# Optimization experiments

Hardware: AMD Instinct MI355X
Metric: run time of the kernel (lower is better)

## Reference

```python
import jax, jax.numpy as jnp
import numpy as np

NEG = -9.0e9  # the -9000000000.0 sentinel used by the torch code


def _masked_bidir_scores(first, second, fmask, smask):
    """Vectorized form of the BxB python double loop in score_grounding.
    first: (B,N,D), second: (B,L,D), fmask: (B,N), smask: (B,L).
    Returns sent_scores (B,B) and mention_scores (B,N,L) (= diagonal att)."""
    mask = fmask[:, None, :, None] * smask[None, :, None, :]          # (B,B,N,L)
    avg = jnp.where(mask != 0, mask, NEG)
    am_first = jax.nn.softmax(avg, axis=2)                            # softmax over N (dim=0 per pair)
    am_second = jax.nn.softmax(avg, axis=3)                           # softmax over L (dim=1 per pair)
    dot = jnp.einsum('ind,jld->ijnl', first, second)                  # (B,B,N,L)
    attm = dot * mask
    att = jnp.where(attm * mask != 0, attm, NEG)
    aw_first = jax.nn.softmax(att, axis=3) * mask                     # softmax(att, dim=-1)*mask
    aw_second = jnp.transpose(
        jax.nn.softmax(jnp.swapaxes(att, 2, 3), axis=3) * jnp.swapaxes(mask, 2, 3), (0, 1, 3, 2)
    )                                                                 # softmax(att.T,-1)*mask.T, transposed back
    sent = (jnp.sum(aw_first * att * am_first, axis=(2, 3))
            + jnp.sum(aw_second * att * am_second, axis=(2, 3)))      # (B,B)
    B = first.shape[0]
    mention = att[jnp.arange(B), jnp.arange(B)]                       # diagonal pairs (B,N,L)
    return sent, mention


def _pairwise_mlp(first, second, W1, b1, W2, b2, W3, b3):
    # SimplePairWiseClassifier: MLP over cat(first, second, first*second); dropout=0 (eval-deterministic)
    x = jnp.concatenate([first, second, first * second], axis=-1)     # (..., 3D)
    h = jax.nn.relu(x @ W1 + b1)
    h = jax.nn.relu(h @ W2 + b2)
    return (h @ W3 + b3)[..., 0]


def setup_inputs() -> dict:
    key = jax.random.key(0)
    ks = jax.random.split(key, 12)
    B, Nt, Ns, L, D, H = 32, 64, 48, 36, 1024, 1024

    def mask(k, n):
        m = (jax.random.uniform(k, (B, n)) < 0.85).astype(jnp.float32)
        return m.at[:, :2].set(1.0)  # guarantee no all-zero rows

    return {
        'text_embeddings': jax.random.normal(ks[0], (B, Nt, D), jnp.float32),
        'span_embeddings': jax.random.normal(ks[1], (B, Ns, D), jnp.float32),
        'image_embeddings': jax.random.normal(ks[2], (B, L, D), jnp.float32),
        'text_mask': mask(ks[3], Nt),
        'span_mask': mask(ks[4], Ns),
        'image_mask': mask(ks[5], L),
        'W1': jax.random.normal(ks[6], (3 * D, H), jnp.float32) * 0.02,
        'b1': jnp.zeros((H,), jnp.float32),
        'W2': jax.random.normal(ks[7], (H, H), jnp.float32) * 0.02,
        'b2': jnp.zeros((H,), jnp.float32),
        'W3': jax.random.normal(ks[8], (H, 1), jnp.float32) * 0.02,
        'b3': jnp.zeros((1,), jnp.float32),
    }


def reference(text_embeddings, span_embeddings, image_embeddings,
              text_mask, span_mask, image_mask, W1, b1, W2, b2, W3, b3):
    B, Ns, D = span_embeddings.shape
    # calculate_loss
    S, _ = _masked_bidir_scores(text_embeddings, image_embeddings, text_mask, image_mask)
    # span_emb.view(B, N, -1, D).mean(dim=2) is identity for (B,Ns,D)
    _, grounding_scores = _masked_bidir_scores(span_embeddings, image_embeddings, span_mask, image_mask)
    # score_text over all span pairs (itertools.combinations order == triu_indices k=1)
    fi, si = np.triu_indices(Ns, k=1)
    text_scores = _pairwise_mlp(span_embeddings[:, fi], span_embeddings[:, si],
                                W1, b1, W2, b2, W3, b3)               # (B, Ns*(Ns-1)/2)
    # contrastive retrieval loss over the BxB sentence-image score matrix
    loss = -(jnp.trace(jax.nn.log_softmax(S, axis=1))
             + jnp.trace(jax.nn.log_softmax(S.T, axis=1))) / B
    return loss, grounding_scores, text_scores
```

## Files before the change

kernel.cpp:

```cpp
#include <hip/hip_runtime.h>
#include <math.h>
#include <stdint.h>

#define B_    32
#define NT    64
#define NS    48
#define LI    36
#define D_    1024
#define H_    1024
#define NPAIR 1128
#define ROWS  (B_*NPAIR)
#define NEGV  -9.0e9f

typedef _Float16 half8 __attribute__((ext_vector_type(8)));
typedef float floatx4 __attribute__((ext_vector_type(4)));
typedef __attribute__((address_space(3))) uint32_t lds_u32;
typedef __attribute__((address_space(1))) const uint32_t glb_u32;

template<int EPI>
__global__ __launch_bounds__(256) void mfma_gemm(
    const _Float16* __restrict__ A, const _Float16* __restrict__ Bt,
    float* __restrict__ Cf, float* __restrict__ scores,
    const float* __restrict__ bias, const float* __restrict__ W3,
    int N, int K, int rowStart) {
  __shared__ __align__(16) _Float16 sA[128 * 32];
  __shared__ __align__(16) _Float16 sB[128 * 32];
  __shared__ float sRed[128][2];
  const int tid = threadIdx.x;
  const int lane = tid & 63;
  const int wave = tid >> 6;
  const int wr = wave >> 1, wc = wave & 1;
  const int l15 = lane & 15, l16 = lane >> 4;
  const int rowBase = blockIdx.y * 128, colBase = blockIdx.x * 128;

  const int stRow = tid >> 2;
  const int stCol = (tid & 3) << 3;
  const _Float16* gA = A + (size_t)(rowBase + stRow) * K + stCol;
  const _Float16* gB = Bt + (size_t)(colBase + stRow) * K + stCol;
  _Float16* lA = sA + tid * 8;
  _Float16* lB = sB + tid * 8;

  floatx4 acc[4][4] = {};
  for (int k0 = 0; k0 < K; k0 += 32) {
    __builtin_amdgcn_global_load_lds((glb_u32*)(gA + k0),           (lds_u32*)lA,             16, 0, 0);
    __builtin_amdgcn_global_load_lds((glb_u32*)(gA + 64 * K + k0),  (lds_u32*)(lA + 64 * 32), 16, 0, 0);
    __builtin_amdgcn_global_load_lds((glb_u32*)(gB + k0),           (lds_u32*)lB,             16, 0, 0);
    __builtin_amdgcn_global_load_lds((glb_u32*)(gB + 64 * K + k0),  (lds_u32*)(lB + 64 * 32), 16, 0, 0);
    __syncthreads();
    half8 aF[4], bF[4];
#pragma unroll
    for (int i = 0; i < 4; ++i)
      aF[i] = *(const half8*)&sA[(wr * 64 + i * 16 + l15) * 32 + l16 * 8];
#pragma unroll
    for (int j = 0; j < 4; ++j)
      bF[j] = *(const half8*)&sB[(wc * 64 + j * 16 + l15) * 32 + l16 * 8];
#pragma unroll
    for (int i = 0; i < 4; ++i)
#pragma unroll
      for (int j = 0; j < 4; ++j)
        acc[i][j] = __builtin_amdgcn_mfma_f32_16x16x32_f16(aF[i], bF[j], acc[i][j], 0, 0, 0);
    __syncthreads();
  }

  if (EPI == 0) {
#pragma unroll
    for (int i = 0; i < 4; ++i)
#pragma unroll
      for (int q = 0; q < 4; ++q) {
        int r = rowBase + wr * 64 + i * 16 + l16 * 4 + q;
#pragma unroll
        for (int j = 0; j < 4; ++j) {
          int c = colBase + wc * 64 + j * 16 + l15;
          Cf[(size_t)r * N + c] = acc[i][j][q];
        }
      }
  } else {
    float bv[4], wv[4];
#pragma unroll
    for (int j = 0; j < 4; ++j) {
      int c = colBase + wc * 64 + j * 16 + l15;
      bv[j] = bias[c];
      wv[j] = W3[c];
    }
#pragma unroll
    for (int i = 0; i < 4; ++i)
#pragma unroll
      for (int q = 0; q < 4; ++q) {
        float s = 0.f;
#pragma unroll
        for (int j = 0; j < 4; ++j) s += fmaxf(acc[i][j][q] + bv[j], 0.f) * wv[j];
        s += __shfl_xor(s, 1); s += __shfl_xor(s, 2);
        s += __shfl_xor(s, 4); s += __shfl_xor(s, 8);
        if (l15 == 0) sRed[wr * 64 + i * 16 + l16 * 4 + q][wc] = s;
      }
    __syncthreads();
    if (tid < 128)
      atomicAdd(&scores[rowStart + rowBase + tid], sRed[tid][0] + sRed[tid][1]);
  }
}

__global__ __launch_bounds__(256) void gemm1_fused(
    const _Float16* __restrict__ spanH, const _Float16* __restrict__ W1cT,
    const float* __restrict__ AB1, const float* __restrict__ b1,
    _Float16* __restrict__ h1out,
    const int* __restrict__ idxF, const int* __restrict__ idxS) {
  __shared__ __align__(16) _Float16 sA[128 * 32];
  __shared__ __align__(16) _Float16 sB[128 * 32];
  __shared__ int sIF[128], sIS[128];
  const int tid = threadIdx.x;
  const int lane = tid & 63;
  const int wave = tid >> 6;
  const int wr = wave >> 1, wc = wave & 1;
  const int l15 = lane & 15, l16 = lane >> 4;
  const int rowBase = blockIdx.y * 128, colBase = blockIdx.x * 128;

  if (tid < 128) {
    int rg = rowBase + tid;
    sIF[tid] = idxF[rg];
    sIS[tid] = idxS[rg];
  }
  __syncthreads();

  const int stRow = tid >> 2;
  const int stCol = (tid & 3) << 3;
  const _Float16* gB = W1cT + (size_t)(colBase + stRow) * D_ + stCol;
  _Float16* lB = sB + tid * 8;
  const size_t pf0 = (size_t)sIF[stRow] * D_;
  const size_t ps0 = (size_t)sIS[stRow] * D_;
  const size_t pf1 = (size_t)sIF[stRow + 64] * D_;
  const size_t ps1 = (size_t)sIS[stRow + 64] * D_;

  floatx4 acc[4][4] = {};
  for (int k0 = 0; k0 < D_; k0 += 32) {
    __builtin_amdgcn_global_load_lds((glb_u32*)(gB + k0),           (lds_u32*)lB,             16, 0, 0);
    __builtin_amdgcn_global_load_lds((glb_u32*)(gB + 64 * D_ + k0), (lds_u32*)(lB + 64 * 32), 16, 0, 0);
    half8 f0 = *(const half8*)(spanH + pf0 + k0 + stCol);
    half8 s0 = *(const half8*)(spanH + ps0 + k0 + stCol);
    half8 f1 = *(const half8*)(spanH + pf1 + k0 + stCol);
    half8 s1 = *(const half8*)(spanH + ps1 + k0 + stCol);
    *(half8*)(sA + stRow * 32 + stCol) = f0 * s0;
    *(half8*)(sA + (stRow + 64) * 32 + stCol) = f1 * s1;
    __syncthreads();
    half8 aF[4], bF[4];
#pragma unroll
    for (int i = 0; i < 4; ++i)
      aF[i] = *(const half8*)&sA[(wr * 64 + i * 16 + l15) * 32 + l16 * 8];
#pragma unroll
    for (int j = 0; j < 4; ++j)
      bF[j] = *(const half8*)&sB[(wc * 64 + j * 16 + l15) * 32 + l16 * 8];
#pragma unroll
    for (int i = 0; i < 4; ++i)
#pragma unroll
      for (int j = 0; j < 4; ++j)
        acc[i][j] = __builtin_amdgcn_mfma_f32_16x16x32_f16(aF[i], bF[j], acc[i][j], 0, 0, 0);
    __syncthreads();
  }

  int cols[4]; float bv[4];
#pragma unroll
  for (int j = 0; j < 4; ++j) {
    cols[j] = colBase + wc * 64 + j * 16 + l15;
    bv[j] = b1[cols[j]];
  }
#pragma unroll
  for (int i = 0; i < 4; ++i)
#pragma unroll
    for (int q = 0; q < 4; ++q) {
      int rL = wr * 64 + i * 16 + l16 * 4 + q;
      int rG = rowBase + rL;
      const float* ap = AB1 + (size_t)sIF[rL] * 2048;
      const float* bp = AB1 + (size_t)sIS[rL] * 2048 + 1024;
#pragma unroll
      for (int j = 0; j < 4; ++j) {
        int c = cols[j];
        float v = acc[i][j][q] + ap[c] + bp[c] + bv[j];
        h1out[(size_t)rG * 1024 + c] = (_Float16)fmaxf(v, 0.f);
      }
    }
}

__global__ __launch_bounds__(256) void cvt_f16(
    const float* __restrict__ in, _Float16* __restrict__ out, long long n8) {
  long long i = (long long)blockIdx.x * 256 + threadIdx.x;
  if (i >= n8) return;
  const float4* p = (const float4*)in + i * 2;
  float4 a = p[0], b = p[1];
  half8 h;
  h[0] = (_Float16)a.x; h[1] = (_Float16)a.y; h[2] = (_Float16)a.z; h[3] = (_Float16)a.w;
  h[4] = (_Float16)b.x; h[5] = (_Float16)b.y; h[6] = (_Float16)b.z; h[7] = (_Float16)b.w;
  *(half8*)(out + i * 8) = h;
}

__global__ __launch_bounds__(256) void transpose_cvt(
    const float* __restrict__ in, _Float16* __restrict__ out) {
  __shared__ float t[32][33];
  const int tx = threadIdx.x & 31, ty = threadIdx.x >> 5;
  const int k0 = blockIdx.y * 32, n0 = blockIdx.x * 32;
#pragma unroll
  for (int q = 0; q < 4; ++q)
    t[ty + q * 8][tx] = in[(size_t)(k0 + ty + q * 8) * 1024 + n0 + tx];
  __syncthreads();
#pragma unroll
  for (int q = 0; q < 4; ++q)
    out[(size_t)(n0 + ty + q * 8) * 1024 + k0 + tx] = (_Float16)t[tx][ty + q * 8];
}

__global__ __launch_bounds__(256) void idx_init(int* __restrict__ idxF, int* __restrict__ idxS) {
  int r = blockIdx.x * 256 + threadIdx.x;
  if (r >= ROWS) return;
  int bb = r / NPAIR, p = r - bb * NPAIR;
  int cum = 0, f = 0;
  while (true) { int cnt = NS - 1 - f; if (p < cum + cnt) break; cum += cnt; ++f; }
  idxF[r] = bb * NS + f;
  idxS[r] = bb * NS + f + 1 + (p - cum);
}

__global__ void init_scores(float* __restrict__ scores, const float* __restrict__ b3) {
  int idx = blockIdx.x * 256 + threadIdx.x;
  if (idx < ROWS) scores[idx] = b3[0];
}

__global__ __launch_bounds__(256) void extract_grounding(
    const float* __restrict__ dotSI, const float* __restrict__ smask,
    const float* __restrict__ imask, float* __restrict__ outg) {
  int idx = blockIdx.x * 256 + threadIdx.x;
  if (idx >= B_ * NS * LI) return;
  int b = idx / (NS * LI);
  int rem = idx - b * (NS * LI);
  int n = rem / LI, l = rem - n * LI;
  float v = dotSI[(size_t)(b * NS + n) * (B_ * LI) + b * LI + l];
  outg[idx] = (smask[b * NS + n] * imask[b * LI + l] != 0.f) ? v : NEGV;
}

__global__ __launch_bounds__(64) void sent_kernel(
    const float* __restrict__ dotTI, const float* __restrict__ tmask,
    const float* __restrict__ imask, float* __restrict__ S) {
  const int i = blockIdx.y, j = blockIdx.x, t = threadIdx.x;
  __shared__ float red1[64], red2[64];
  const int stride = B_ * LI;
  float e1 = 0.f;
  {
    float tm = tmask[i * NT + t];
    if (tm != 0.f) {
      const float* row = dotTI + (size_t)(i * NT + t) * stride + j * LI;
      float m = -INFINITY;
      for (int l = 0; l < LI; ++l) if (imask[j * LI + l] != 0.f) m = fmaxf(m, row[l]);
      float z = 0.f, w = 0.f;
      for (int l = 0; l < LI; ++l) if (imask[j * LI + l] != 0.f) {
        float d = row[l], p = expf(d - m);
        z += p; w += p * d;
      }
      e1 = w / z;
    }
  }
  red1[t] = e1;
  float e2 = 0.f;
  if (t < LI) {
    float im = imask[j * LI + t];
    if (im != 0.f) {
      const float* col = dotTI + (size_t)(i * NT) * stride + j * LI + t;
      float m = -INFINITY;
      for (int n = 0; n < NT; ++n) if (tmask[i * NT + n] != 0.f) m = fmaxf(m, col[(size_t)n * stride]);
      float z = 0.f, w = 0.f;
      for (int n = 0; n < NT; ++n) if (tmask[i * NT + n] != 0.f) {
        float d = col[(size_t)n * stride], p = expf(d - m);
        z += p; w += p * d;
      }
      e2 = w / z;
    }
  }
  red2[t] = e2;
  __syncthreads();
  if (t == 0) {
    float s1 = 0.f, s2 = 0.f, cn = 0.f, cl = 0.f;
    for (int n = 0; n < NT; ++n) { s1 += red1[n]; cn += tmask[i * NT + n]; }
    for (int l = 0; l < LI; ++l) { s2 += red2[l]; cl += imask[j * LI + l]; }
    S[i * B_ + j] = s1 / cn + s2 / cl;
  }
}

__global__ __launch_bounds__(64) void loss_kernel(
    const float* __restrict__ S, float* __restrict__ out) {
  __shared__ float sS[B_][B_ + 1];
  __shared__ float acc[B_];
  const int t = threadIdx.x;
  for (int e = t; e < B_ * B_; e += 64) sS[e / B_][e % B_] = S[e];
  __syncthreads();
  if (t < B_) {
    float m = -INFINITY;
    for (int j = 0; j < B_; ++j) m = fmaxf(m, sS[t][j]);
    float z = 0.f;
    for (int j = 0; j < B_; ++j) z += expf(sS[t][j] - m);
    float lr = m + logf(z);
    float m2 = -INFINITY;
    for (int i = 0; i < B_; ++i) m2 = fmaxf(m2, sS[i][t]);
    float z2 = 0.f;
    for (int i = 0; i < B_; ++i) z2 += expf(sS[i][t] - m2);
    float lc = m2 + logf(z2);
    acc[t] = 2.f * sS[t][t] - lr - lc;
  }
  __syncthreads();
  if (t == 0) {
    float s = 0.f;
    for (int i = 0; i < B_; ++i) s += acc[i];
    out[0] = -s / (float)B_;
  }
}

extern "C" void kernel_launch(void* const* d_in, const int* in_sizes, int n_in,
                              void* d_out, int out_size, void* d_ws, size_t ws_size,
                              hipStream_t stream) {
  const float* text  = (const float*)d_in[0];
  const float* span  = (const float*)d_in[1];
  const float* img   = (const float*)d_in[2];
  const float* tmask = (const float*)d_in[3];
  const float* smask = (const float*)d_in[4];
  const float* imask = (const float*)d_in[5];
  const float* W1    = (const float*)d_in[6];
  const float* b1    = (const float*)d_in[7];
  const float* W2    = (const float*)d_in[8];
  const float* b2    = (const float*)d_in[9];
  const float* W3    = (const float*)d_in[10];
  const float* b3    = (const float*)d_in[11];

  float* out     = (float*)d_out;
  float* outLoss = out;
  float* outG    = out + 1;
  float* outT    = out + 1 + (size_t)B_ * NS * LI;

  char* w = (char*)d_ws;
  float*    dotTI = (float*)w;            w += (size_t)(B_*NT) * (B_*LI) * 4;
  float*    dotSI = (float*)w;            w += (size_t)(B_*NS) * (B_*LI) * 4;
  float*    S     = (float*)w;            w += 1024 * 4;
  float*    AB1   = (float*)w;            w += (size_t)1536 * 2048 * 4;
  _Float16* h1    = (_Float16*)w;         w += (size_t)ROWS * 1024 * 2;
  _Float16* textH = (_Float16*)w;         w += (size_t)2048 * 1024 * 2;
  _Float16* spanH = (_Float16*)w;         w += (size_t)1536 * 1024 * 2;
  _Float16* imgH  = (_Float16*)w;         w += (size_t)1152 * 1024 * 2;
  _Float16* W1abT = (_Float16*)w;         w += (size_t)2048 * 1024 * 2;
  _Float16* W1cT  = (_Float16*)w;         w += (size_t)1024 * 1024 * 2;
  _Float16* W2T   = (_Float16*)w;         w += (size_t)1024 * 1024 * 2;
  int*      idxF  = (int*)w;              w += ROWS * 4;
  int*      idxS  = (int*)w;              w += ROWS * 4;
  (void)ws_size; (void)in_sizes; (void)n_in; (void)out_size;

  cvt_f16<<<(2048 * 128 + 255) / 256, 256, 0, stream>>>(text, textH, 2048LL * 128);
  cvt_f16<<<(1536 * 128 + 255) / 256, 256, 0, stream>>>(span, spanH, 1536LL * 128);
  cvt_f16<<<(1152 * 128 + 255) / 256, 256, 0, stream>>>(img, imgH, 1152LL * 128);
  transpose_cvt<<<dim3(32, 32), 256, 0, stream>>>(W1, W1abT);
  transpose_cvt<<<dim3(32, 32), 256, 0, stream>>>(W1 + 1024 * 1024, W1abT + 1024 * 1024);
  transpose_cvt<<<dim3(32, 32), 256, 0, stream>>>(W1 + 2048 * 1024, W1cT);
  transpose_cvt<<<dim3(32, 32), 256, 0, stream>>>(W2, W2T);
  idx_init<<<(ROWS + 255) / 256, 256, 0, stream>>>(idxF, idxS);

  mfma_gemm<0><<<dim3((B_*LI) / 128, (B_*NT) / 128), 256, 0, stream>>>(
      textH, imgH, dotTI, nullptr, nullptr, nullptr, B_ * LI, D_, 0);
  sent_kernel<<<dim3(B_, B_), 64, 0, stream>>>(dotTI, tmask, imask, S);
  loss_kernel<<<1, 64, 0, stream>>>(S, outLoss);

  mfma_gemm<0><<<dim3((B_*LI) / 128, (B_*NS) / 128), 256, 0, stream>>>(
      spanH, imgH, dotSI, nullptr, nullptr, nullptr, B_ * LI, D_, 0);
  extract_grounding<<<(B_*NS*LI + 255) / 256, 256, 0, stream>>>(dotSI, smask, imask, outG);

  mfma_gemm<0><<<dim3(2048 / 128, 1536 / 128), 256, 0, stream>>>(
      spanH, W1abT, AB1, nullptr, nullptr, nullptr, 2048, D_, 0);

  gemm1_fused<<<dim3(1024 / 128, ROWS / 128), 256, 0, stream>>>(
      spanH, W1cT, AB1, b1, h1, idxF, idxS);

  init_scores<<<(ROWS + 255) / 256, 256, 0, stream>>>(outT, b3);
  mfma_gemm<2><<<dim3(1024 / 128, ROWS / 128), 256, 0, stream>>>(
      h1, W2T, nullptr, outT, b2, W3, 1024, H_, 0);
}
```

Measured before the change: 385.9 us.

## Double K-step per barrier and remap blocks to XCD-contiguous row tiles

GEMM main loops now load a 64-wide K slab per iteration as two 32-wide halves, halving the number of barriers and load-issue rounds per tile. The two large MLP GEMMs switch to a 1D grid whose block IDs are remapped so each XCD processes a contiguous band of row tiles across all column tiles, aiming to improve L2 locality of the A operand. LDS use per block doubles, which may reduce occupancy, and a few padding blocks exit early.

```diff
diff --git a/kernel.cpp b/kernel.cpp
--- a/kernel.cpp
+++ b/kernel.cpp
@@ -11,54 +11,76 @@
 #define NPAIR 1128
 #define ROWS  (B_*NPAIR)
 #define NEGV  -9.0e9f
+#define NROWT 282
+#define CPX   36
 
 typedef _Float16 half8 __attribute__((ext_vector_type(8)));
 typedef float floatx4 __attribute__((ext_vector_type(4)));
 typedef __attribute__((address_space(3))) uint32_t lds_u32;
 typedef __attribute__((address_space(1))) const uint32_t glb_u32;
 
-template<int EPI>
+#define GLOAD16(src, dst) __builtin_amdgcn_global_load_lds((glb_u32*)(src), (lds_u32*)(dst), 16, 0, 0)
+
+template<int EPI, int REMAP>
 __global__ __launch_bounds__(256) void mfma_gemm(
     const _Float16* __restrict__ A, const _Float16* __restrict__ Bt,
     float* __restrict__ Cf, float* __restrict__ scores,
     const float* __restrict__ bias, const float* __restrict__ W3,
-    int N, int K, int rowStart) {
-  __shared__ __align__(16) _Float16 sA[128 * 32];
-  __shared__ __align__(16) _Float16 sB[128 * 32];
+    int N, int K) {
+  __shared__ __align__(16) _Float16 sA[8192];
+  __shared__ __align__(16) _Float16 sB[8192];
   __shared__ float sRed[128][2];
+  int rowT, colT;
+  if (REMAP) {
+    int bid = blockIdx.x;
+    int x = bid & 7, ord = bid >> 3;
+    rowT = x * CPX + (ord >> 3);
+    colT = ord & 7;
+    if (rowT >= NROWT) return;
+  } else {
+    rowT = blockIdx.y; colT = blockIdx.x;
+  }
+  const int rowBase = rowT * 128, colBase = colT * 128;
   const int tid = threadIdx.x;
   const int lane = tid & 63;
   const int wave = tid >> 6;
   const int wr = wave >> 1, wc = wave & 1;
   const int l15 = lane & 15, l16 = lane >> 4;
-  const int rowBase = blockIdx.y * 128, colBase = blockIdx.x * 128;
-
-  const int stRow = tid >> 2;
-  const int stCol = (tid & 3) << 3;
-  const _Float16* gA = A + (size_t)(rowBase + stRow) * K + stCol;
-  const _Float16* gB = Bt + (size_t)(colBase + stRow) * K + stCol;
+
+  const int sRow = tid >> 2;
+  const int sCol = (tid & 3) << 3;
+  const _Float16* gA = A + (size_t)(rowBase + sRow) * K + sCol;
+  const _Float16* gB = Bt + (size_t)(colBase + sRow) * K + sCol;
   _Float16* lA = sA + tid * 8;
   _Float16* lB = sB + tid * 8;
 
   floatx4 acc[4][4] = {};
-  for (int k0 = 0; k0 < K; k0 += 32) {
-    __builtin_amdgcn_global_load_lds((glb_u32*)(gA + k0),           (lds_u32*)lA,             16, 0, 0);
-    __builtin_amdgcn_global_load_lds((glb_u32*)(gA + 64 * K + k0),  (lds_u32*)(lA + 64 * 32), 16, 0, 0);
-    __builtin_amdgcn_global_load_lds((glb_u32*)(gB + k0),           (lds_u32*)lB,             16, 0, 0);
-    __builtin_amdgcn_global_load_lds((glb_u32*)(gB + 64 * K + k0),  (lds_u32*)(lB + 64 * 32), 16, 0, 0);
+  for (int k0 = 0; k0 < K; k0 += 64) {
+    GLOAD16(gA + k0,              lA);
+    GLOAD16(gA + 64 * K + k0,     lA + 2048);
+    GLOAD16(gA + k0 + 32,         lA + 4096);
+    GLOAD16(gA + 64 * K + k0 + 32,lA + 6144);
+    GLOAD16(gB + k0,              lB);
+    GLOAD16(gB + 64 * K + k0,     lB + 2048);
+    GLOAD16(gB + k0 + 32,         lB + 4096);
+    GLOAD16(gB + 64 * K + k0 + 32,lB + 6144);
     __syncthreads();
-    half8 aF[4], bF[4];
-#pragma unroll
-    for (int i = 0; i < 4; ++i)
-      aF[i] = *(const half8*)&sA[(wr * 64 + i * 16 + l15) * 32 + l16 * 8];
-#pragma unroll
-    for (int j = 0; j < 4; ++j)
-      bF[j] = *(const half8*)&sB[(wc * 64 + j * 16 + l15) * 32 + l16 * 8];
-#pragma unroll
-    for (int i = 0; i < 4; ++i)
+#pragma unroll
+    for (int h = 0; h < 2; ++h) {
+      const int hb = h * 4096;
+      half8 aF[4], bF[4];
+#pragma unroll
+      for (int i = 0; i < 4; ++i)
+        aF[i] = *(const half8*)&sA[hb + (wr * 64 + i * 16 + l15) * 32 + l16 * 8];
 #pragma unroll
       for (int j = 0; j < 4; ++j)
-        acc[i][j] = __builtin_amdgcn_mfma_f32_16x16x32_f16(aF[i], bF[j], acc[i][j], 0, 0, 0);
+        bF[j] = *(const half8*)&sB[hb + (wc * 64 + j * 16 + l15) * 32 + l16 * 8];
+#pragma unroll
+      for (int i = 0; i < 4; ++i)
+#pragma unroll
+        for (int j = 0; j < 4; ++j)
+          acc[i][j] = __builtin_amdgcn_mfma_f32_16x16x32_f16(aF[i], bF[j], acc[i][j], 0, 0, 0);
+    }
     __syncthreads();
   }
 
@@ -95,7 +117,7 @@
       }
     __syncthreads();
     if (tid < 128)
-      atomicAdd(&scores[rowStart + rowBase + tid], sRed[tid][0] + sRed[tid][1]);
+      atomicAdd(&scores[rowBase + tid], sRed[tid][0] + sRed[tid][1]);
   }
 }
 
@@ -104,15 +126,20 @@
     const float* __restrict__ AB1, const float* __restrict__ b1,
     _Float16* __restrict__ h1out,
     const int* __restrict__ idxF, const int* __restrict__ idxS) {
-  __shared__ __align__(16) _Float16 sA[128 * 32];
-  __shared__ __align__(16) _Float16 sB[128 * 32];
+  __shared__ __align__(16) _Float16 sA[8192];
+  __shared__ __align__(16) _Float16 sB[8192];
   __shared__ int sIF[128], sIS[128];
+  int bid = blockIdx.x;
+  int x = bid & 7, ord = bid >> 3;
+  int rowT = x * CPX + (ord >> 3);
+  int colT = ord & 7;
+  if (rowT >= NROWT) return;
+  const int rowBase = rowT * 128, colBase = colT * 128;
   const int tid = threadIdx.x;
   const int lane = tid & 63;
   const int wave = tid >> 6;
   const int wr = wave >> 1, wc = wave & 1;
   const int l15 = lane & 15, l16 = lane >> 4;
-  const int rowBase = blockIdx.y * 128, colBase = blockIdx.x * 128;
 
   if (tid < 128) {
     int rg = rowBase + tid;
@@ -121,38 +148,50 @@
   }
   __syncthreads();
 
-  const int stRow = tid >> 2;
-  const int stCol = (tid & 3) << 3;
-  const _Float16* gB = W1cT + (size_t)(colBase + stRow) * D_ + stCol;
+  const int sRow = tid >> 2;
+  const int sCol = (tid & 3) << 3;
+  const _Float16* gB = W1cT + (size_t)(colBase + sRow) * D_ + sCol;
   _Float16* lB = sB + tid * 8;
-  const size_t pf0 = (size_t)sIF[stRow] * D_;
-  const size_t ps0 = (size_t)sIS[stRow] * D_;
-  const size_t pf1 = (size_t)sIF[stRow + 64] * D_;
-  const size_t ps1 = (size_t)sIS[stRow + 64] * D_;
+  const _Float16* pf0 = spanH + (size_t)sIF[sRow] * D_ + sCol;
+  const _Float16* ps0 = spanH + (size_t)sIS[sRow] * D_ + sCol;
+  const _Float16* pf1 = spanH + (size_t)sIF[sRow + 64] * D_ + sCol;
+  const _Float16* ps1 = spanH + (size_t)sIS[sRow + 64] * D_ + sCol;
 
   floatx4 acc[4][4] = {};
-  for (int k0 = 0; k0 < D_; k0 += 32) {
-    __builtin_amdgcn_global_load_lds((glb_u32*)(gB + k0),           (lds_u32*)lB,             16, 0, 0);
-    __builtin_amdgcn_global_load_lds((glb_u32*)(gB + 64 * D_ + k0), (lds_u32*)(lB + 64 * 32), 16, 0, 0);
-    half8 f0 = *(const half8*)(spanH + pf0 + k0 + stCol);
-    half8 s0 = *(const half8*)(spanH + ps0 + k0 + stCol);
-    half8 f1 = *(const half8*)(spanH + pf1 + k0 + stCol);
-    half8 s1 = *(const half8*)(spanH + ps1 + k0 + stCol);
-    *(half8*)(sA + stRow * 32 + stCol) = f0 * s0;
-    *(half8*)(sA + (stRow + 64) * 32 + stCol) = f1 * s1;
+  for (int k0 = 0; k0 < D_; k0 += 64) {
+    GLOAD16(gB + k0,               lB);
+    GLOAD16(gB + 64 * D_ + k0,     lB + 2048);
+    GLOAD16(gB + k0 + 32,          lB + 4096);
+    GLOAD16(gB + 64 * D_ + k0 + 32,lB + 6144);
+    half8 f00 = *(const half8*)(pf0 + k0);
+    half8 s00 = *(const half8*)(ps0 + k0);
+    half8 f10 = *(const half8*)(pf1 + k0);
+    half8 s10 = *(const half8*)(ps1 + k0);
+    half8 f01 = *(const half8*)(pf0 + k0 + 32);
+    half8 s01 = *(const half8*)(ps0 + k0 + 32);
+    half8 f11 = *(const half8*)(pf1 + k0 + 32);
+    half8 s11 = *(const half8*)(ps1 + k0 + 32);
+    *(half8*)(sA + tid * 8)        = f00 * s00;
+    *(half8*)(sA + 2048 + tid * 8) = f10 * s10;
+    *(half8*)(sA + 4096 + tid * 8) = f01 * s01;
+    *(half8*)(sA + 6144 + tid * 8) = f11 * s11;
     __syncthreads();
-    half8 aF[4], bF[4];
-#pragma unroll
-    for (int i = 0; i < 4; ++i)
-      aF[i] = *(const half8*)&sA[(wr * 64 + i * 16 + l15) * 32 + l16 * 8];
-#pragma unroll
-    for (int j = 0; j < 4; ++j)
-      bF[j] = *(const half8*)&sB[(wc * 64 + j * 16 + l15) * 32 + l16 * 8];
-#pragma unroll
-    for (int i = 0; i < 4; ++i)
+#pragma unroll
+    for (int h = 0; h < 2; ++h) {
+      const int hb = h * 4096;
+      half8 aF[4], bF[4];
+#pragma unroll
+      for (int i = 0; i < 4; ++i)
+        aF[i] = *(const half8*)&sA[hb + (wr * 64 + i * 16 + l15) * 32 + l16 * 8];
 #pragma unroll
       for (int j = 0; j < 4; ++j)
-        acc[i][j] = __builtin_amdgcn_mfma_f32_16x16x32_f16(aF[i], bF[j], acc[i][j], 0, 0, 0);
+        bF[j] = *(const half8*)&sB[hb + (wc * 64 + j * 16 + l15) * 32 + l16 * 8];
+#pragma unroll
+      for (int i = 0; i < 4; ++i)
+#pragma unroll
+        for (int j = 0; j < 4; ++j)
+          acc[i][j] = __builtin_amdgcn_mfma_f32_16x16x32_f16(aF[i], bF[j], acc[i][j], 0, 0, 0);
+    }
     __syncthreads();
   }
 
@@ -353,22 +392,22 @@
   transpose_cvt<<<dim3(32, 32), 256, 0, stream>>>(W2, W2T);
   idx_init<<<(ROWS + 255) / 256, 256, 0, stream>>>(idxF, idxS);
 
-  mfma_gemm<0><<<dim3((B_*LI) / 128, (B_*NT) / 128), 256, 0, stream>>>(
-      textH, imgH, dotTI, nullptr, nullptr, nullptr, B_ * LI, D_, 0);
+  mfma_gemm<0, 0><<<dim3((B_*LI) / 128, (B_*NT) / 128), 256, 0, stream>>>(
+      textH, imgH, dotTI, nullptr, nullptr, nullptr, B_ * LI, D_);
   sent_kernel<<<dim3(B_, B_), 64, 0, stream>>>(dotTI, tmask, imask, S);
   loss_kernel<<<1, 64, 0, stream>>>(S, outLoss);
 
-  mfma_gemm<0><<<dim3((B_*LI) / 128, (B_*NS) / 128), 256, 0, stream>>>(
-      spanH, imgH, dotSI, nullptr, nullptr, nullptr, B_ * LI, D_, 0);
+  mfma_gemm<0, 0><<<dim3((B_*LI) / 128, (B_*NS) / 128), 256, 0, stream>>>(
+      spanH, imgH, dotSI, nullptr, nullptr, nullptr, B_ * LI, D_);
   extract_grounding<<<(B_*NS*LI + 255) / 256, 256, 0, stream>>>(dotSI, smask, imask, outG);
 
-  mfma_gemm<0><<<dim3(2048 / 128, 1536 / 128), 256, 0, stream>>>(
-      spanH, W1abT, AB1, nullptr, nullptr, nullptr, 2048, D_, 0);
-
-  gemm1_fused<<<dim3(1024 / 128, ROWS / 128), 256, 0, stream>>>(
+  mfma_gemm<0, 0><<<dim3(2048 / 128, 1536 / 128), 256, 0, stream>>>(
+      spanH, W1abT, AB1, nullptr, nullptr, nullptr, 2048, D_);
+
+  gemm1_fused<<<8 * CPX * 8, 256, 0, stream>>>(
       spanH, W1cT, AB1, b1, h1, idxF, idxS);
 
   init_scores<<<(ROWS + 255) / 256, 256, 0, stream>>>(outT, b3);
-  mfma_gemm<2><<<dim3(1024 / 128, ROWS / 128), 256, 0, stream>>>(
-      h1, W2T, nullptr, outT, b2, W3, 1024, H_, 0);
-}
+  mfma_gemm<2, 1><<<8 * CPX * 8, 256, 0, stream>>>(
+      h1, W2T, nullptr, outT, b2, W3, 1024, H_);
+}
```

Result: faster. 362.8 us (-6.0%).
